# Optimization experiments

Hardware: AMD Instinct MI355X
Metric: run time of the kernel (lower is better)

The kernel has to match this reference:

```python
import jax, jax.numpy as jnp
import numpy as np

B, C, I, S = 16384, 64, 9, 10        # nodes, channels(num_features), irreps_in dim, num_species
K = {3: 23, 2: 5, 1: 2}              # CG path counts per correlation order
U_DENSITY = 0.1                      # CG-like sparsity of the U tensors


def _make_U(key, shape):
    k1, k2 = jax.random.split(key)
    vals = jax.random.normal(k1, shape, dtype=jnp.float32)
    mask = jax.random.bernoulli(k2, U_DENSITY, shape)
    return jnp.where(mask, vals, 0.0)


def setup_inputs() -> dict:
    key = jax.random.key(0)
    ks = jax.random.split(key, 16)
    x = jax.random.normal(ks[0], (B, C, I), dtype=jnp.float32)
    species = jax.random.randint(ks[1], (B,), 0, S)
    y = jax.nn.one_hot(species, S, dtype=jnp.float32)  # (B, S) one-hot node attrs
    # scalar (0e) output: U_nu shape = (I,)*nu + (k,)
    U3_s = _make_U(ks[2], (I, I, I, K[3]))
    U2_s = _make_U(ks[3], (I, I, K[2]))
    U1_s = _make_U(ks[4], (I, K[1]))
    # vector (1o) output: U_nu shape = (3,) + (I,)*nu + (k,)
    U3_v = _make_U(ks[5], (3, I, I, I, K[3]))
    U2_v = _make_U(ks[6], (3, I, I, K[2]))
    U1_v = _make_U(ks[7], (3, I, K[1]))
    def w(k, nparams):
        return jax.random.normal(k, (S, nparams, C), dtype=jnp.float32) / jnp.sqrt(float(nparams))
    W3_s, W2_s, W1_s = w(ks[8], K[3]), w(ks[9], K[2]), w(ks[10], K[1])
    W3_v, W2_v, W1_v = w(ks[11], K[3]), w(ks[12], K[2]), w(ks[13], K[1])
    return {"x": x, "y": y,
            "U3_s": U3_s, "U2_s": U2_s, "U1_s": U1_s,
            "W3_s": W3_s, "W2_s": W2_s, "W1_s": W1_s,
            "U3_v": U3_v, "U2_v": U2_v, "U1_v": U1_v,
            "W3_v": W3_v, "W2_v": W2_v, "W1_v": W1_v}


def _contraction(x, y, U3, U2, U1, W3, W2, W1):
    # correlation-3 element-dependent contraction (MACE Contraction.__call__)
    # main: '...ik,ekc,bci,be -> bc...'
    out = jnp.einsum('...ik,ekc,bci,be->bc...', U3, W3, x, y)
    # corr = 2: weighting '...k,ekc,be->bc...' then contract 'bc...i,bci->bc...'
    c = jnp.einsum('...k,ekc,be->bc...', U2, W2, y) + out
    out = jnp.einsum('bc...i,bci->bc...', c, x)
    # corr = 1
    c = jnp.einsum('...k,ekc,be->bc...', U1, W1, y) + out
    out = jnp.einsum('bc...i,bci->bc...', c, x)
    return out.reshape(out.shape[0], -1)  # flatten trailing dims


def reference(x, y, U3_s, U2_s, U1_s, W3_s, W2_s, W1_s,
              U3_v, U2_v, U1_v, W3_v, W2_v, W1_v):
    out_s = _contraction(x, y, U3_s, U2_s, U1_s, W3_s, W2_s, W1_s)  # (B, C)
    out_v = _contraction(x, y, U3_v, U2_v, U1_v, W3_v, W2_v, W1_v)  # (B, 3*C)
    return jnp.concatenate([out_s, out_v], axis=-1)  # (B, 4*C)
```

## Files before the change

kernel.cpp:

```cpp
#include <hip/hip_runtime.h>
#include <cstdint>

#define B_NODES 16384
#define C_CH    64
#define I_DIM   9
#define S_SPEC  10
#define K3C     23
#define K2C     5
#define K1C     2
#define NTRI    165
#define NPAIR   45
#define NSING   9
#define NIDX    (NTRI + NPAIR + NSING)
#define TILE_N  256
#define MAXT    74
#define NROUND  10
#define SCAP    (MAXT * TILE_N)
#define OUT_STRIDE (4 * C_CH)
#define NHB     32

#define N3SL (NTRI * K3C)
#define N2SL (NPAIR * K2C)
#define N1SL (NSING * K1C)
#define NUSYM (N3SL + N2SL + N1SL)

typedef float v2f __attribute__((ext_vector_type(2)));
typedef float v4f __attribute__((ext_vector_type(4)));


__global__ __launch_bounds__(256) void k_prep(
        const float* __restrict__ y,
        const float* __restrict__ U3s, const float* __restrict__ U2s,
        const float* __restrict__ U1s,
        const float* __restrict__ U3v, const float* __restrict__ U2v,
        const float* __restrict__ U1v,
        int* __restrict__ species, int* __restrict__ cnt,
        float* __restrict__ us3, float* __restrict__ uv3,
        float* __restrict__ us2, float* __restrict__ uv2,
        float* __restrict__ us1, float* __restrict__ uv1) {
    int tid = threadIdx.x;
    if (blockIdx.x < NHB) {
        __shared__ int hcnt[S_SPEC];
        if (tid < S_SPEC) hcnt[tid] = 0;
        __syncthreads();
        int chunk = B_NODES / NHB;
        int base = blockIdx.x * chunk;
        for (int i = base + tid; i < base + chunk; i += 256) {
            int e = 0; float best = -1.f;
            #pragma unroll
            for (int j = 0; j < S_SPEC; ++j) {
                float v = y[i * S_SPEC + j];
                if (v > best) { best = v; e = j; }
            }
            species[i] = e;
            atomicAdd(&hcnt[e], 1);
        }
        __syncthreads();
        if (tid < S_SPEC && hcnt[tid] > 0) atomicAdd(&cnt[tid], hcnt[tid]);
        return;
    }
    int t = (blockIdx.x - NHB) * 256 + tid;
    if (t >= NUSYM) return;

    if (t < N3SL) {
        int idx = t / K3C, k = t % K3C;
        int p = 0, q = 0, r = 0, cum = 0;
        for (int p0 = 0; p0 < 9; ++p0)
            for (int q0 = p0; q0 < 9; ++q0)
                for (int r0 = q0; r0 < 9; ++r0) {
                    if (cum == idx) { p = p0; q = q0; r = r0; }
                    ++cum;
                }
        int perm[6][3] = {{p,q,r},{p,r,q},{q,p,r},{q,r,p},{r,p,q},{r,q,p}};
        float a0 = 0.f, a1 = 0.f, a2 = 0.f, a3 = 0.f;
        for (int j = 0; j < 6; ++j) {
            bool dup = false;
            for (int j2 = 0; j2 < j; ++j2)
                if (perm[j2][0]==perm[j][0] && perm[j2][1]==perm[j][1] && perm[j2][2]==perm[j][2])
                    dup = true;
            if (dup) continue;
            int a = perm[j][0], bb = perm[j][1], i = perm[j][2];
            int off = ((a * 9 + bb) * 9 + i) * K3C + k;
            a0 += U3s[off];
            a1 += U3v[0 * 729 * K3C + off];
            a2 += U3v[1 * 729 * K3C + off];
            a3 += U3v[2 * 729 * K3C + off];
        }
        us3[t] = a0;
        uv3[0 * N3SL + t] = a1;
        uv3[1 * N3SL + t] = a2;
        uv3[2 * N3SL + t] = a3;
    } else if (t < N3SL + N2SL) {
        int t2 = t - N3SL;
        int idx = t2 / K2C, k = t2 % K2C;
        int p = 0, q = 0, cum = 0;
        for (int p0 = 0; p0 < 9; ++p0)
            for (int q0 = p0; q0 < 9; ++q0) {
                if (cum == idx) { p = p0; q = q0; }
                ++cum;
            }
        int np = (p == q) ? 1 : 2;
        int pa[2] = {p, q}, pb[2] = {q, p};
        float a0 = 0.f, a1 = 0.f, a2 = 0.f, a3 = 0.f;
        for (int j = 0; j < np; ++j) {
            int off = (pa[j] * 9 + pb[j]) * K2C + k;
            a0 += U2s[off];
            a1 += U2v[0 * 81 * K2C + off];
            a2 += U2v[1 * 81 * K2C + off];
            a3 += U2v[2 * 81 * K2C + off];
        }
        us2[t2] = a0;
        uv2[0 * N2SL + t2] = a1;
        uv2[1 * N2SL + t2] = a2;
        uv2[2 * N2SL + t2] = a3;
    } else {
        int t1 = t - N3SL - N2SL;
        us1[t1] = U1s[t1];
        uv1[0 * N1SL + t1] = U1v[0 * 9 * K1C + t1];
        uv1[1 * N1SL + t1] = U1v[1 * 9 * K1C + t1];
        uv1[2 * N1SL + t1] = U1v[2 * 9 * K1C + t1];
    }
}


__global__ __launch_bounds__(256) void k_plan(
        const int* __restrict__ cnt, int* __restrict__ seg_start,
        int* __restrict__ cursor, int* __restrict__ tilesp, int* __restrict__ sorted) {
    int tid = threadIdx.x;
    int gtid = blockIdx.x * 256 + tid;
    for (int i = gtid; i < SCAP; i += NHB * 256) sorted[i] = -1;
    if (blockIdx.x == 0) {
        if (tid < MAXT) tilesp[tid] = -1;
        __syncthreads();
        if (tid == 0) {
            int run = 0;
            for (int e = 0; e < S_SPEC; ++e) {
                seg_start[e] = run;
                cursor[e] = 0;
                int tiles = (cnt[e] + TILE_N - 1) / TILE_N;
                for (int t = 0; t < tiles; ++t) tilesp[run / TILE_N + t] = e;
                run += tiles * TILE_N;
            }
        }
    }
}


__global__ __launch_bounds__(256) void k_mid(
        const int* __restrict__ species, const int* __restrict__ seg_start,
        int* __restrict__ cursor, int* __restrict__ sorted,
        const float* __restrict__ W3s, const float* __restrict__ W2s,
        const float* __restrict__ W1s,
        const float* __restrict__ W3v, const float* __restrict__ W2v,
        const float* __restrict__ W1v,
        const float* __restrict__ us3, const float* __restrict__ uv3,
        const float* __restrict__ us2, const float* __restrict__ uv2,
        const float* __restrict__ us1, const float* __restrict__ uv1,
        float* __restrict__ table) {
    int tid = threadIdx.x;
    if (blockIdx.x < B_NODES / 256) {
        int b = blockIdx.x * 256 + tid;
        int e = species[b];
        int lane = tid & 63;
        unsigned long long lanebit = 1ull << lane;
        for (int j = 0; j < S_SPEC; ++j) {
            unsigned long long m = __ballot(e == j);
            if (m == 0ull) continue;
            int leader = __ffsll(m) - 1;
            int base = 0;
            if (lane == leader) base = atomicAdd(&cursor[j], __popcll(m));
            base = __shfl(base, leader);
            if (e == j) {
                int pos = base + __popcll(m & (lanebit - 1ull));
                sorted[seg_start[j] + pos] = b;
            }
        }
        return;
    }
    int t = (blockIdx.x - B_NODES / 256) * 256 + tid;
    int m   = t & 3;
    int row = (t >> 2) % NIDX;
    int ec  = t / (4 * NIDX);
    int c = ec & (C_CH - 1), e = ec >> 6;

    int type = -1, pp = 0, pidx = 0, tidx = 0;
    {
        int cum = 0, pcount = 0, tcount = 0;
        for (int p0 = 0; p0 < 9; ++p0) {
            if (cum == row) { type = 0; pp = p0; }
            ++cum;
            for (int q0 = p0; q0 < 9; ++q0) {
                if (cum == row) { type = 1; pidx = pcount; }
                ++cum; ++pcount;
                for (int r0 = q0; r0 < 9; ++r0) {
                    if (cum == row) { type = 2; tidx = tcount; }
                    ++cum; ++tcount;
                }
            }
        }
    }

    const float* up; const float* Wb; int K;
    if (type == 2) {
        K = K3C;
        up = (m == 0) ? (us3 + tidx * K3C) : (uv3 + (size_t)(m - 1) * N3SL + tidx * K3C);
        Wb = ((m == 0) ? W3s : W3v) + (size_t)e * K3C * C_CH + c;
    } else if (type == 1) {
        K = K2C;
        up = (m == 0) ? (us2 + pidx * K2C) : (uv2 + (size_t)(m - 1) * N2SL + pidx * K2C);
        Wb = ((m == 0) ? W2s : W2v) + (size_t)e * K2C * C_CH + c;
    } else {
        K = K1C;
        up = (m == 0) ? (us1 + pp * K1C) : (uv1 + (size_t)(m - 1) * N1SL + pp * K1C);
        Wb = ((m == 0) ? W1s : W1v) + (size_t)e * K1C * C_CH + c;
    }
    float acc = 0.f;
    for (int k = 0; k < K; ++k) acc += up[k] * Wb[k * C_CH];
    table[t] = acc;
}


__global__ __launch_bounds__(256) void k_main(
        const float* __restrict__ x, const float* __restrict__ table,
        const int* __restrict__ sorted, const int* __restrict__ tilesp,
        float* __restrict__ out) {
    __shared__ float xs[TILE_N * 9];
    __shared__ v4f   ts[NIDX];

    int f = blockIdx.x;
    int xcd = f & 7;
    int j = f >> 3;
    int t = (j >> 6) * 8 + xcd;
    int c = j & 63;
    if (t >= MAXT) return;
    int e = tilesp[t];
    if (e < 0) return;
    int tid = threadIdx.x;

    const v4f* __restrict__ Tg = (const v4f*)table + (size_t)(e * C_CH + c) * NIDX;
    if (tid < NIDX) ts[tid] = Tg[tid];

    for (int s = tid; s < TILE_N * 9; s += 256) {
        int n = s / 9, i = s - n * 9;
        int b = sorted[t * TILE_N + n];
        float v = (b >= 0) ? x[((size_t)b * C_CH + c) * I_DIM + i] : 0.f;
        xs[n * 9 + i] = v;
    }
    __syncthreads();

    float xr[9];
    #pragma unroll
    for (int i = 0; i < 9; ++i) xr[i] = xs[tid * 9 + i];

    v2f a01 = {0.f, 0.f}, a23 = {0.f, 0.f};
    int tix = 0;
    #pragma unroll
    for (int p = 0; p < 9; ++p) {
        {
            v4f rs = ts[tix]; ++tix;
            a01 += (v2f){rs[0], rs[1]} * xr[p];
            a23 += (v2f){rs[2], rs[3]} * xr[p];
        }
        #pragma unroll
        for (int q = p; q < 9; ++q) {
            float m2 = xr[p] * xr[q];
            v4f rp = ts[tix]; ++tix;
            a01 += (v2f){rp[0], rp[1]} * m2;
            a23 += (v2f){rp[2], rp[3]} * m2;
            #pragma unroll
            for (int r = q; r < 9; ++r) {
                float m3 = m2 * xr[r];
                v4f rt = ts[tix]; ++tix;
                a01 += (v2f){rt[0], rt[1]} * m3;
                a23 += (v2f){rt[2], rt[3]} * m3;
            }
        }
    }

    int b = sorted[t * TILE_N + tid];
    if (b < 0) return;
    out[(size_t)b * OUT_STRIDE + c] = a01.x;
    float* ov = out + (size_t)b * OUT_STRIDE + C_CH + c * 3;
    ov[0] = a01.y; ov[1] = a23.x; ov[2] = a23.y;
}


extern "C" void kernel_launch(void* const* d_in, const int* in_sizes, int n_in,
                              void* d_out, int out_size, void* d_ws, size_t ws_size,
                              hipStream_t stream) {
    const float* x   = (const float*)d_in[0];
    const float* y   = (const float*)d_in[1];
    const float* U3s = (const float*)d_in[2];
    const float* U2s = (const float*)d_in[3];
    const float* U1s = (const float*)d_in[4];
    const float* W3s = (const float*)d_in[5];
    const float* W2s = (const float*)d_in[6];
    const float* W1s = (const float*)d_in[7];
    const float* U3v = (const float*)d_in[8];
    const float* U2v = (const float*)d_in[9];
    const float* U1v = (const float*)d_in[10];
    const float* W3v = (const float*)d_in[11];
    const float* W2v = (const float*)d_in[12];
    const float* W1v = (const float*)d_in[13];
    float* out = (float*)d_out;

    char* ws = (char*)d_ws;
    size_t off = 0;
    auto alloc = [&](size_t bytes) -> char* {
        char* p = ws + off;
        off = (off + bytes + 255) & ~(size_t)255;
        return p;
    };
    float* table   = (float*)alloc((size_t)S_SPEC * C_CH * NIDX * 4 * sizeof(float));
    float* us3     = (float*)alloc(N3SL * sizeof(float));
    float* uv3     = (float*)alloc(3 * N3SL * sizeof(float));
    float* us2     = (float*)alloc(N2SL * sizeof(float));
    float* uv2     = (float*)alloc(3 * N2SL * sizeof(float));
    float* us1     = (float*)alloc(N1SL * sizeof(float));
    float* uv1     = (float*)alloc(3 * N1SL * sizeof(float));
    int* sorted    = (int*)alloc(SCAP * sizeof(int));
    int* tilesp    = (int*)alloc(MAXT * sizeof(int));
    int* species   = (int*)alloc(B_NODES * sizeof(int));
    int* seg_start = (int*)alloc(S_SPEC * sizeof(int));
    int* cursor    = (int*)alloc(S_SPEC * sizeof(int));
    int* cnt       = (int*)alloc(S_SPEC * sizeof(int));

    hipMemsetAsync(cnt, 0, S_SPEC * sizeof(int), stream);

    int prep_blocks = NHB + (NUSYM + 255) / 256;
    hipLaunchKernelGGL(k_prep, dim3(prep_blocks), dim3(256), 0, stream,
                       y, U3s, U2s, U1s, U3v, U2v, U1v,
                       species, cnt,
                       us3, uv3, us2, uv2, us1, uv1);

    hipLaunchKernelGGL(k_plan, dim3(NHB), dim3(256), 0, stream,
                       cnt, seg_start, cursor, tilesp, sorted);

    int table_threads = S_SPEC * C_CH * NIDX * 4;
    int mid_blocks = B_NODES / 256 + table_threads / 256;
    hipLaunchKernelGGL(k_mid, dim3(mid_blocks), dim3(256), 0, stream,
                       species, seg_start, cursor, sorted,
                       W3s, W2s, W1s, W3v, W2v, W1v,
                       us3, uv3, us2, uv2, us1, uv1, table);

    hipLaunchKernelGGL(k_main, dim3(NROUND * 8 * 64), dim3(256), 0, stream,
                       x, table, sorted, tilesp, out);
}
```

Baseline: 108.8 us.

## Drop plan kernel by deriving segments from counts inline and memset sorted

Removes the k_plan launch. Segment offsets are now computed on the fly from species counts in k_mid, and k_main finds its species tile by scanning the counts instead of reading a tilesp table. The sorted buffer is initialised with a memset, and the cursor zeroing is merged into the existing count memset. The U symmetrisation threads are also split four ways, one output component each, to spread the prep work over more threads. The aim is to cut one kernel launch and its serial single-thread plan step, at the cost of small redundant count loops in every thread.

```diff
diff --git a/kernel.cpp b/kernel.cpp
--- a/kernel.cpp
+++ b/kernel.cpp
@@ -59,8 +59,10 @@
         if (tid < S_SPEC && hcnt[tid] > 0) atomicAdd(&cnt[tid], hcnt[tid]);
         return;
     }
-    int t = (blockIdx.x - NHB) * 256 + tid;
-    if (t >= NUSYM) return;
+    int tt = (blockIdx.x - NHB) * 256 + tid;
+    if (tt >= 4 * NUSYM) return;
+    int m = tt / NUSYM;
+    int t = tt - m * NUSYM;
 
     if (t < N3SL) {
         int idx = t / K3C, k = t % K3C;
@@ -71,8 +73,9 @@
                     if (cum == idx) { p = p0; q = q0; r = r0; }
                     ++cum;
                 }
+        const float* src = (m == 0) ? U3s : (U3v + (size_t)(m - 1) * 729 * K3C);
         int perm[6][3] = {{p,q,r},{p,r,q},{q,p,r},{q,r,p},{r,p,q},{r,q,p}};
-        float a0 = 0.f, a1 = 0.f, a2 = 0.f, a3 = 0.f;
+        float a0 = 0.f;
         for (int j = 0; j < 6; ++j) {
             bool dup = false;
             for (int j2 = 0; j2 < j; ++j2)
@@ -80,16 +83,10 @@
                     dup = true;
             if (dup) continue;
             int a = perm[j][0], bb = perm[j][1], i = perm[j][2];
-            int off = ((a * 9 + bb) * 9 + i) * K3C + k;
-            a0 += U3s[off];
-            a1 += U3v[0 * 729 * K3C + off];
-            a2 += U3v[1 * 729 * K3C + off];
-            a3 += U3v[2 * 729 * K3C + off];
-        }
-        us3[t] = a0;
-        uv3[0 * N3SL + t] = a1;
-        uv3[1 * N3SL + t] = a2;
-        uv3[2 * N3SL + t] = a3;
+            a0 += src[((a * 9 + bb) * 9 + i) * K3C + k];
+        }
+        float* dst = (m == 0) ? us3 : (uv3 + (size_t)(m - 1) * N3SL);
+        dst[t] = a0;
     } else if (t < N3SL + N2SL) {
         int t2 = t - N3SL;
         int idx = t2 / K2C, k = t2 % K2C;
@@ -99,55 +96,22 @@
                 if (cum == idx) { p = p0; q = q0; }
                 ++cum;
             }
-        int np = (p == q) ? 1 : 2;
-        int pa[2] = {p, q}, pb[2] = {q, p};
-        float a0 = 0.f, a1 = 0.f, a2 = 0.f, a3 = 0.f;
-        for (int j = 0; j < np; ++j) {
-            int off = (pa[j] * 9 + pb[j]) * K2C + k;
-            a0 += U2s[off];
-            a1 += U2v[0 * 81 * K2C + off];
-            a2 += U2v[1 * 81 * K2C + off];
-            a3 += U2v[2 * 81 * K2C + off];
-        }
-        us2[t2] = a0;
-        uv2[0 * N2SL + t2] = a1;
-        uv2[1 * N2SL + t2] = a2;
-        uv2[2 * N2SL + t2] = a3;
+        const float* src = (m == 0) ? U2s : (U2v + (size_t)(m - 1) * 81 * K2C);
+        float a0 = src[(p * 9 + q) * K2C + k];
+        if (p != q) a0 += src[(q * 9 + p) * K2C + k];
+        float* dst = (m == 0) ? us2 : (uv2 + (size_t)(m - 1) * N2SL);
+        dst[t2] = a0;
     } else {
         int t1 = t - N3SL - N2SL;
-        us1[t1] = U1s[t1];
-        uv1[0 * N1SL + t1] = U1v[0 * 9 * K1C + t1];
-        uv1[1 * N1SL + t1] = U1v[1 * 9 * K1C + t1];
-        uv1[2 * N1SL + t1] = U1v[2 * 9 * K1C + t1];
+        const float* src = (m == 0) ? U1s : (U1v + (size_t)(m - 1) * 9 * K1C);
+        float* dst = (m == 0) ? us1 : (uv1 + (size_t)(m - 1) * N1SL);
+        dst[t1] = src[t1];
     }
 }
 
 
-__global__ __launch_bounds__(256) void k_plan(
-        const int* __restrict__ cnt, int* __restrict__ seg_start,
-        int* __restrict__ cursor, int* __restrict__ tilesp, int* __restrict__ sorted) {
-    int tid = threadIdx.x;
-    int gtid = blockIdx.x * 256 + tid;
-    for (int i = gtid; i < SCAP; i += NHB * 256) sorted[i] = -1;
-    if (blockIdx.x == 0) {
-        if (tid < MAXT) tilesp[tid] = -1;
-        __syncthreads();
-        if (tid == 0) {
-            int run = 0;
-            for (int e = 0; e < S_SPEC; ++e) {
-                seg_start[e] = run;
-                cursor[e] = 0;
-                int tiles = (cnt[e] + TILE_N - 1) / TILE_N;
-                for (int t = 0; t < tiles; ++t) tilesp[run / TILE_N + t] = e;
-                run += tiles * TILE_N;
-            }
-        }
-    }
-}
-
-
 __global__ __launch_bounds__(256) void k_mid(
-        const int* __restrict__ species, const int* __restrict__ seg_start,
+        const int* __restrict__ species, const int* __restrict__ cnt,
         int* __restrict__ cursor, int* __restrict__ sorted,
         const float* __restrict__ W3s, const float* __restrict__ W2s,
         const float* __restrict__ W1s,
@@ -163,17 +127,20 @@
         int e = species[b];
         int lane = tid & 63;
         unsigned long long lanebit = 1ull << lane;
+        int runseg = 0;
         for (int j = 0; j < S_SPEC; ++j) {
             unsigned long long m = __ballot(e == j);
-            if (m == 0ull) continue;
-            int leader = __ffsll(m) - 1;
-            int base = 0;
-            if (lane == leader) base = atomicAdd(&cursor[j], __popcll(m));
-            base = __shfl(base, leader);
-            if (e == j) {
-                int pos = base + __popcll(m & (lanebit - 1ull));
-                sorted[seg_start[j] + pos] = b;
-            }
+            if (m != 0ull) {
+                int leader = __ffsll(m) - 1;
+                int base = 0;
+                if (lane == leader) base = atomicAdd(&cursor[j], __popcll(m));
+                base = __shfl(base, leader);
+                if (e == j) {
+                    int pos = base + __popcll(m & (lanebit - 1ull));
+                    sorted[runseg + pos] = b;
+                }
+            }
+            runseg += ((cnt[j] + TILE_N - 1) / TILE_N) * TILE_N;
         }
         return;
     }
@@ -222,7 +189,7 @@
 
 __global__ __launch_bounds__(256) void k_main(
         const float* __restrict__ x, const float* __restrict__ table,
-        const int* __restrict__ sorted, const int* __restrict__ tilesp,
+        const int* __restrict__ sorted, const int* __restrict__ cnt,
         float* __restrict__ out) {
     __shared__ float xs[TILE_N * 9];
     __shared__ v4f   ts[NIDX];
@@ -232,8 +199,13 @@
     int j = f >> 3;
     int t = (j >> 6) * 8 + xcd;
     int c = j & 63;
-    if (t >= MAXT) return;
-    int e = tilesp[t];
+    int e = -1, run = 0;
+    #pragma unroll
+    for (int s = 0; s < S_SPEC; ++s) {
+        int tiles = (cnt[s] + TILE_N - 1) / TILE_N;
+        if (t >= run && t < run + tiles) e = s;
+        run += tiles;
+    }
     if (e < 0) return;
     int tid = threadIdx.x;
 
@@ -319,30 +291,27 @@
     float* us1     = (float*)alloc(N1SL * sizeof(float));
     float* uv1     = (float*)alloc(3 * N1SL * sizeof(float));
     int* sorted    = (int*)alloc(SCAP * sizeof(int));
-    int* tilesp    = (int*)alloc(MAXT * sizeof(int));
     int* species   = (int*)alloc(B_NODES * sizeof(int));
-    int* seg_start = (int*)alloc(S_SPEC * sizeof(int));
-    int* cursor    = (int*)alloc(S_SPEC * sizeof(int));
-    int* cnt       = (int*)alloc(S_SPEC * sizeof(int));
-
-    hipMemsetAsync(cnt, 0, S_SPEC * sizeof(int), stream);
-
-    int prep_blocks = NHB + (NUSYM + 255) / 256;
+    int* cntcur    = (int*)alloc(2 * S_SPEC * sizeof(int));
+    int* cnt       = cntcur;
+    int* cursor    = cntcur + S_SPEC;
+
+    hipMemsetAsync(cntcur, 0, 2 * S_SPEC * sizeof(int), stream);
+    hipMemsetAsync(sorted, 0xFF, SCAP * sizeof(int), stream);
+
+    int prep_blocks = NHB + (4 * NUSYM + 255) / 256;
     hipLaunchKernelGGL(k_prep, dim3(prep_blocks), dim3(256), 0, stream,
                        y, U3s, U2s, U1s, U3v, U2v, U1v,
                        species, cnt,
                        us3, uv3, us2, uv2, us1, uv1);
 
-    hipLaunchKernelGGL(k_plan, dim3(NHB), dim3(256), 0, stream,
-                       cnt, seg_start, cursor, tilesp, sorted);
-
     int table_threads = S_SPEC * C_CH * NIDX * 4;
     int mid_blocks = B_NODES / 256 + table_threads / 256;
     hipLaunchKernelGGL(k_mid, dim3(mid_blocks), dim3(256), 0, stream,
-                       species, seg_start, cursor, sorted,
+                       species, cnt, cursor, sorted,
                        W3s, W2s, W1s, W3v, W2v, W1v,
                        us3, uv3, us2, uv2, us1, uv1, table);
 
     hipLaunchKernelGGL(k_main, dim3(NROUND * 8 * 64), dim3(256), 0, stream,
-                       x, table, sorted, tilesp, out);
+                       x, table, sorted, cnt, out);
 }
```

New measurement: 101.1 us. 7.0% less time.
